# Optimization experiments

Hardware: AMD Instinct MI355X
Metric: run time of the kernel (lower is better)

Reference implementation:

```python
import jax, jax.numpy as jnp
import numpy as np

B, C, Q, E = 32, 1024, 128, 512

def setup_inputs() -> dict:
    key = jax.random.key(0)
    k1, k2, k3 = jax.random.split(key, 3)
    context = jax.random.normal(k1, (B, C, E), dtype=jnp.float32)
    question = jax.random.normal(k2, (B, Q, E), dtype=jnp.float32)
    # ws = [ws_q | ws_c | ws_m], matching cat([q, ctx, q*ctx]) order
    ws = jax.random.normal(k3, (3 * E,), dtype=jnp.float32) * (1.0 / np.sqrt(E))
    return {"context": context, "question": question, "ws": ws}

def reference(context, question, ws):
    ws_q, ws_c, ws_m = ws[:E], ws[E:2 * E], ws[2 * E:]
    # similarity[b,c,q] = ws_q.q[b,q] + ws_c.c[b,c] + ws_m.(q[b,q]*c[b,c])
    sim = (jnp.einsum('bqe,e->bq', question, ws_q)[:, None, :]
           + jnp.einsum('bce,e->bc', context, ws_c)[:, :, None]
           + jnp.einsum('bce,bqe,e->bcq', context, question, ws_m))  # (B,C,Q)
    c2q = jnp.einsum('bcq,bqe->bce', jax.nn.softmax(sim, axis=2), question)  # (B,C,E)
    q2c_w = jax.nn.softmax(jnp.max(sim, axis=2), axis=1)  # (B,C)
    q2c = jnp.einsum('bc,bce->be', q2c_w, context)[:, None, :]  # (B,1,E)
    return (c2q, q2c)
```

## Files before the change

kernel.cpp:

```cpp
#include <hip/hip_runtime.h>

#define BB 32
#define CC 1024
#define QQ 128
#define EE 512

typedef unsigned int uint32;
typedef unsigned short u16;
typedef __bf16 bf16x8 __attribute__((ext_vector_type(8)));
typedef float f32x4 __attribute__((ext_vector_type(4)));

#define QMF_OFF  (0u)
#define QTF_OFF  (4u<<20)
#define QDP_OFF  (8u<<20)
#define RDEN_OFF ((8u<<20)+(1u<<16))
#define MB_OFF   ((8u<<20)+(3u<<16))
#define SB_OFF   ((8u<<20)+(3u<<16)+4096u)
#define PVB_OFF  ((8u<<20)+(4u<<16))
#define P_OFF    (11u<<20)

__device__ __forceinline__ u16 bfc(float f){
  __bf16 h = (__bf16)f;
  return __builtin_bit_cast(u16, h);
}
__device__ __forceinline__ float bf2f(uint32 lo16){
  return __builtin_bit_cast(float, lo16 << 16);
}

__global__ __launch_bounds__(256) void k_prep(const float* __restrict__ q,
                                              const float* __restrict__ ws,
                                              unsigned char* __restrict__ wsp){
  const int b = blockIdx.x >> 2, et = blockIdx.x & 3, e0 = et*128;
  __shared__ u16 tm[128*136];
  __shared__ u16 tt[128*136];
  const int tid = threadIdx.x;
  float* qdp = (float*)(wsp + QDP_OFF) + (size_t)(b*4 + et)*128;
  #pragma unroll
  for (int i=0;i<16;i++){
    int id = tid + i*256;
    int qi = id >> 5;
    int el = (id & 31) << 2;
    float4 v = *(const float4*)(q + (size_t)(b*QQ+qi)*EE + e0 + el);
    float4 a = *(const float4*)(ws +          e0 + el);
    float4 c = *(const float4*)(ws +   EE +   e0 + el);
    float4 m = *(const float4*)(ws + 2*EE +   e0 + el);
    ushort4 um; um.x = bfc(v.x*m.x + c.x); um.y = bfc(v.y*m.y + c.y);
                um.z = bfc(v.z*m.z + c.z); um.w = bfc(v.w*m.w + c.w);
    *(ushort4*)&tm[qi*136 + el] = um;
    ushort4 ut; ut.x = bfc(v.x); ut.y = bfc(v.y); ut.z = bfc(v.z); ut.w = bfc(v.w);
    *(ushort4*)&tt[qi*136 + el] = ut;
    float d = v.x*a.x + v.y*a.y + v.z*a.z + v.w*a.w;
    d += __shfl_xor(d,1); d += __shfl_xor(d,2); d += __shfl_xor(d,4);
    d += __shfl_xor(d,8); d += __shfl_xor(d,16);
    if ((tid & 31) == 0) qdp[qi] = d;
  }
  __syncthreads();
  const int lane = tid & 63, wv = tid >> 6, l15 = lane & 15, l4 = lane >> 4;
  uint4* qmf = (uint4*)(wsp + QMF_OFF);
  uint4* qtf = (uint4*)(wsp + QTF_OFF);
  #pragma unroll
  for (int i=0;i<8;i++){
    int f = wv*8 + i;
    int kl = f >> 3, nf = f & 7;
    uint4 u = *(const uint4*)&tm[(nf*16 + l15)*136 + kl*32 + l4*8];
    qmf[(size_t)((b*16 + et*4 + kl)*8 + nf)*64 + lane] = u;
  }
  #pragma unroll
  for (int i=0;i<8;i++){
    int f = wv*8 + i;
    int ks2 = f >> 3, nl = f & 7, ne = et*8 + nl;
    uint32 x[4];
    #pragma unroll
    for (int p=0;p<4;p++){
      u16 t0 = tt[(ks2*32 + l4*8 + 2*p    )*136 + nl*16 + l15];
      u16 t1 = tt[(ks2*32 + l4*8 + 2*p + 1)*136 + nl*16 + l15];
      x[p] = (uint32)t0 | ((uint32)t1 << 16);
    }
    uint4 u; u.x = x[0]; u.y = x[1]; u.z = x[2]; u.w = x[3];
    qtf[(size_t)((b*4 + ks2)*32 + ne)*64 + lane] = u;
  }
}

__global__ __launch_bounds__(512, 4) void k_sim(const float* __restrict__ ctx,
                                                unsigned char* __restrict__ wsp){
  __shared__ __align__(16) unsigned char buf[32768];
  __shared__ float mx_s[32*8];
  __shared__ float sm_s[32*8];
  __shared__ float wrow_s[32];

  const int bid = blockIdx.x;
  const int sw  = (bid & 7)*128 + (bid >> 3);
  const int b   = sw >> 5;
  const int t   = sw & 31;
  const int tid = threadIdx.x;
  const int lane = tid & 63;
  const int w    = tid >> 6;
  const int l15  = lane & 15;
  const int l4   = lane >> 4;

  const float4* cb4 = (const float4*)(ctx + (size_t)(b*CC + t*32)*EE);
  float4 v[8];
  #pragma unroll
  for (int i=0;i<8;i++) v[i] = cb4[i*512 + tid];

  const uint4* qmf4 = (const uint4*)(wsp + QMF_OFF);
  bf16x8 a[16];
  #pragma unroll
  for (int ks=0;ks<16;ks++)
    a[ks] = __builtin_bit_cast(bf16x8, qmf4[(size_t)((b*16 + ks)*8 + w)*64 + lane]);
  float qdv[4];
  {
    const float* qdp = (const float*)(wsp + QDP_OFF) + (size_t)b*512;
    #pragma unroll
    for (int r=0;r<4;r++){
      const int qi = w*16 + l4*4 + r;
      qdv[r] = qdp[qi] + qdp[128+qi] + qdp[256+qi] + qdp[384+qi];
    }
  }

  {
    const int colb = (tid & 127)*8;
    #pragma unroll
    for (int i=0;i<8;i++){
      const int row = i*4 + (tid >> 7);
      uint2 u;
      u.x = (uint32)bfc(v[i].x) | ((uint32)bfc(v[i].y) << 16);
      u.y = (uint32)bfc(v[i].z) | ((uint32)bfc(v[i].w) << 16);
      *(uint2*)(buf + row*1024 + (colb ^ ((row & 7) << 4))) = u;
    }
  }
  __syncthreads();

  f32x4 acc[2];
  acc[0] = (f32x4){0.f,0.f,0.f,0.f};
  acc[1] = (f32x4){0.f,0.f,0.f,0.f};
  #pragma unroll
  for (int ks=0; ks<16; ks++){
    #pragma unroll
    for (int cc=0; cc<2; cc++){
      const int row = cc*16 + l15;
      bf16x8 bf = __builtin_bit_cast(bf16x8,
        *(const uint4*)(buf + row*1024 + ((ks*64 + l4*16) ^ ((row & 7) << 4))));
      acc[cc] = __builtin_amdgcn_mfma_f32_16x16x32_bf16(a[ks], bf, acc[cc], 0, 0, 0);
    }
  }

  {
    unsigned char* pgb = wsp + P_OFF
      + ((size_t)(b*64 + t*2)*4 + (w>>1))*1024
      + (((2*w + (l4>>1)) & 3)*16 + l15)*16 + (l4&1)*8;
    #pragma unroll
    for (int cc=0; cc<2; cc++){
      float m = -3.0e38f, s = 0.f;
      u16 hb[4];
      #pragma unroll
      for (int r=0;r<4;r++){
        float vv = fminf(acc[cc][r] + qdv[r], 80.f);
        m = fmaxf(m, vv);
        u16 h = bfc(__expf(vv));
        hb[r] = h;
        s += bf2f(h);
      }
      uint2 u; u.x = (uint32)hb[0] | ((uint32)hb[1]<<16);
               u.y = (uint32)hb[2] | ((uint32)hb[3]<<16);
      *(uint2*)(pgb + cc*4096) = u;
      m = fmaxf(m, __shfl_xor(m, 16)); m = fmaxf(m, __shfl_xor(m, 32));
      s += __shfl_xor(s, 16);          s += __shfl_xor(s, 32);
      if (l4 == 0){
        mx_s[(cc*16 + l15)*8 + w] = m;
        sm_s[(cc*16 + l15)*8 + w] = s;
      }
    }
  }
  __syncthreads();

  if (tid < 32){
    const float* sp = &sm_s[tid*8];
    float sum = sp[0]+sp[1]+sp[2]+sp[3]+sp[4]+sp[5]+sp[6]+sp[7];
    ((float*)(wsp + RDEN_OFF))[b*1024 + t*32 + tid] = 1.f/sum;
    const float* mp = &mx_s[tid*8];
    float mf = fmaxf(fmaxf(fmaxf(mp[0],mp[1]),fmaxf(mp[2],mp[3])),
                     fmaxf(fmaxf(mp[4],mp[5]),fmaxf(mp[6],mp[7])));
    float M = mf;
    M = fmaxf(M, __shfl_xor(M,1)); M = fmaxf(M, __shfl_xor(M,2));
    M = fmaxf(M, __shfl_xor(M,4)); M = fmaxf(M, __shfl_xor(M,8));
    M = fmaxf(M, __shfl_xor(M,16));
    float wr = __expf(mf - M);
    wrow_s[tid] = wr;
    float S = wr;
    S += __shfl_xor(S,1); S += __shfl_xor(S,2); S += __shfl_xor(S,4);
    S += __shfl_xor(S,8); S += __shfl_xor(S,16);
    if (tid == 0){
      ((float*)(wsp + MB_OFF))[b*32 + t] = M;
      ((float*)(wsp + SB_OFF))[b*32 + t] = S;
    }
  }
  __syncthreads();

  {
    float pv = 0.f;
    #pragma unroll
    for (int rr=0; rr<32; rr++){
      uint32 x = *(const u16*)(buf + rr*1024 + ((tid*2) ^ ((rr & 7) << 4)));
      pv = fmaf(wrow_s[rr], bf2f(x), pv);
    }
    ((float*)(wsp + PVB_OFF))[(size_t)(b*32 + t)*512 + tid] = pv;
  }
}

__global__ __launch_bounds__(256, 4) void k_out(unsigned char* __restrict__ wsp,
                                                float* __restrict__ out){
  __shared__ __align__(16) unsigned char qts[32768];

  const int bid = blockIdx.x;
  const int sw  = (bid & 7)*256 + (bid >> 3);
  const int b   = sw >> 6;
  const int rr  = sw & 63;
  const int ct  = rr >> 2;
  const int et  = rr & 3;
  const int tid = threadIdx.x;
  const int lane = tid & 63;
  const int w    = tid >> 6;
  const int l15  = lane & 15;
  const int l4   = lane >> 4;

  const unsigned char* qtfb = wsp + QTF_OFF + (size_t)b*131072;
  #pragma unroll
  for (int j=0;j<8;j++){
    __builtin_amdgcn_global_load_lds(
      (const __attribute__((address_space(1))) uint32*)
        (qtfb + (size_t)(w*32 + et*8 + j)*1024 + lane*16),
      (__attribute__((address_space(3))) uint32*)(qts + (w*8 + j)*1024), 16, 0, 0);
  }

  bf16x8 pa[4];
  #pragma unroll
  for (int k2=0;k2<4;k2++)
    pa[k2] = __builtin_bit_cast(bf16x8,
      *(const uint4*)(wsp + P_OFF + ((size_t)(b*64 + ct*4 + w)*4 + k2)*1024 + lane*16));
  float rden[4];
  {
    const float* rg = (const float*)(wsp + RDEN_OFF) + b*1024 + ct*64 + w*16;
    #pragma unroll
    for (int r=0;r<4;r++) rden[r] = rg[l4*4 + r];
  }
  __syncthreads();

  f32x4 acc2[8];
  #pragma unroll
  for (int n=0;n<8;n++) acc2[n] = (f32x4){0.f,0.f,0.f,0.f};
  #pragma unroll
  for (int k2=0;k2<4;k2++){
    #pragma unroll
    for (int n=0;n<8;n++){
      bf16x8 bq = __builtin_bit_cast(bf16x8,
        *(const uint4*)(qts + (k2*8 + n)*1024 + lane*16));
      acc2[n] = __builtin_amdgcn_mfma_f32_16x16x32_bf16(pa[k2], bq, acc2[n], 0, 0, 0);
    }
  }

  float* ob = out + (size_t)(b*CC + ct*64 + w*16)*EE + et*128;
  #pragma unroll
  for (int n=0;n<8;n++){
    #pragma unroll
    for (int r=0;r<4;r++)
      ob[(size_t)(l4*4 + r)*EE + n*16 + l15] = acc2[n][r]*rden[r];
  }
}

__global__ __launch_bounds__(256) void k_fin(unsigned char* __restrict__ wsp,
                                             float* __restrict__ out){
  const int b = blockIdx.x;
  __shared__ float sc_s[32];
  __shared__ float dinv_s;
  const int tid = threadIdx.x;
  if (tid < 32){
    float Mk = ((const float*)(wsp + MB_OFF))[b*32 + tid];
    float Sk = ((const float*)(wsp + SB_OFF))[b*32 + tid];
    float M = Mk;
    M = fmaxf(M, __shfl_xor(M,1)); M = fmaxf(M, __shfl_xor(M,2));
    M = fmaxf(M, __shfl_xor(M,4)); M = fmaxf(M, __shfl_xor(M,8));
    M = fmaxf(M, __shfl_xor(M,16));
    float ev = __expf(Mk - M);
    float d = ev*Sk;
    d += __shfl_xor(d,1); d += __shfl_xor(d,2); d += __shfl_xor(d,4);
    d += __shfl_xor(d,8); d += __shfl_xor(d,16);
    sc_s[tid] = ev;
    if (tid == 0) dinv_s = 1.f/d;
  }
  __syncthreads();
  const float* pvb = (const float*)(wsp + PVB_OFF) + (size_t)b*32*512;
  float a0 = 0.f, a1 = 0.f;
  #pragma unroll
  for (int k=0;k<32;k++){
    float s = sc_s[k];
    a0 = fmaf(s, pvb[k*512 + tid],       a0);
    a1 = fmaf(s, pvb[k*512 + tid + 256], a1);
  }
  size_t base = (size_t)BB*CC*EE + (size_t)b*EE;
  float di = dinv_s;
  out[base + tid]       = a0*di;
  out[base + tid + 256] = a1*di;
}

extern "C" void kernel_launch(void* const* d_in, const int* in_sizes, int n_in,
                              void* d_out, int out_size, void* d_ws, size_t ws_size,
                              hipStream_t stream){
  const float* ctx = (const float*)d_in[0];
  const float* q   = (const float*)d_in[1];
  const float* ws  = (const float*)d_in[2];
  float* out = (float*)d_out;
  unsigned char* wsp = (unsigned char*)d_ws;

  k_prep<<<dim3(BB*4), dim3(256), 0, stream>>>(q, ws, wsp);
  k_sim <<<dim3(1024), dim3(512), 0, stream>>>(ctx, wsp);
  k_out <<<dim3(2048), dim3(256), 0, stream>>>(wsp, out);
  k_fin <<<dim3(BB),   dim3(256), 0, stream>>>(wsp, out);
}
```

Before: 53.56 us.

## Halve k_sim context tile to 16 rows and fold k_fin into k_out

```diff
diff --git a/kernel.cpp b/kernel.cpp
--- a/kernel.cpp
+++ b/kernel.cpp
@@ -13,11 +13,11 @@
 #define QMF_OFF  (0u)
 #define QTF_OFF  (4u<<20)
 #define QDP_OFF  (8u<<20)
-#define RDEN_OFF ((8u<<20)+(1u<<16))
-#define MB_OFF   ((8u<<20)+(3u<<16))
-#define SB_OFF   ((8u<<20)+(3u<<16)+4096u)
-#define PVB_OFF  ((8u<<20)+(4u<<16))
-#define P_OFF    (11u<<20)
+#define RDEN_OFF ((8u<<20)+(64u<<10))
+#define MB_OFF   ((8u<<20)+(192u<<10))
+#define SB_OFF   ((8u<<20)+(200u<<10))
+#define PVB_OFF  ((8u<<20)+(256u<<10))
+#define P_OFF    (13u<<20)
 
 __device__ __forceinline__ u16 bfc(float f){
   __bf16 h = (__bf16)f;
@@ -83,31 +83,26 @@
 
 __global__ __launch_bounds__(512, 4) void k_sim(const float* __restrict__ ctx,
                                                 unsigned char* __restrict__ wsp){
-  __shared__ __align__(16) unsigned char buf[32768];
-  __shared__ float mx_s[32*8];
-  __shared__ float sm_s[32*8];
-  __shared__ float wrow_s[32];
+  __shared__ __align__(16) unsigned char buf[16384];
+  __shared__ float mx_s[16*8];
+  __shared__ float sm_s[16*8];
+  __shared__ float wrow_s[16];
 
   const int bid = blockIdx.x;
-  const int sw  = (bid & 7)*128 + (bid >> 3);
-  const int b   = sw >> 5;
-  const int t   = sw & 31;
+  const int sw  = (bid & 7)*256 + (bid >> 3);
+  const int b   = sw >> 6;
+  const int t   = sw & 63;
   const int tid = threadIdx.x;
   const int lane = tid & 63;
   const int w    = tid >> 6;
   const int l15  = lane & 15;
   const int l4   = lane >> 4;
 
-  const float4* cb4 = (const float4*)(ctx + (size_t)(b*CC + t*32)*EE);
-  float4 v[8];
-  #pragma unroll
-  for (int i=0;i<8;i++) v[i] = cb4[i*512 + tid];
-
-  const uint4* qmf4 = (const uint4*)(wsp + QMF_OFF);
-  bf16x8 a[16];
-  #pragma unroll
-  for (int ks=0;ks<16;ks++)
-    a[ks] = __builtin_bit_cast(bf16x8, qmf4[(size_t)((b*16 + ks)*8 + w)*64 + lane]);
+  const float4* cb4 = (const float4*)(ctx + (size_t)(b*CC + t*16)*EE);
+  float4 v[4];
+  #pragma unroll
+  for (int i=0;i<4;i++) v[i] = cb4[i*512 + tid];
+
   float qdv[4];
   {
     const float* qdp = (const float*)(wsp + QDP_OFF) + (size_t)b*512;
@@ -121,7 +116,7 @@
   {
     const int colb = (tid & 127)*8;
     #pragma unroll
-    for (int i=0;i<8;i++){
+    for (int i=0;i<4;i++){
       const int row = i*4 + (tid >> 7);
       uint2 u;
       u.x = (uint32)bfc(v[i].x) | ((uint32)bfc(v[i].y) << 16);
@@ -131,68 +126,56 @@
   }
   __syncthreads();
 
-  f32x4 acc[2];
-  acc[0] = (f32x4){0.f,0.f,0.f,0.f};
-  acc[1] = (f32x4){0.f,0.f,0.f,0.f};
+  const uint4* qmf4 = (const uint4*)(wsp + QMF_OFF);
+  f32x4 acc = (f32x4){0.f,0.f,0.f,0.f};
   #pragma unroll
   for (int ks=0; ks<16; ks++){
-    #pragma unroll
-    for (int cc=0; cc<2; cc++){
-      const int row = cc*16 + l15;
-      bf16x8 bf = __builtin_bit_cast(bf16x8,
-        *(const uint4*)(buf + row*1024 + ((ks*64 + l4*16) ^ ((row & 7) << 4))));
-      acc[cc] = __builtin_amdgcn_mfma_f32_16x16x32_bf16(a[ks], bf, acc[cc], 0, 0, 0);
-    }
-  }
-
-  {
-    unsigned char* pgb = wsp + P_OFF
-      + ((size_t)(b*64 + t*2)*4 + (w>>1))*1024
-      + (((2*w + (l4>>1)) & 3)*16 + l15)*16 + (l4&1)*8;
-    #pragma unroll
-    for (int cc=0; cc<2; cc++){
-      float m = -3.0e38f, s = 0.f;
-      u16 hb[4];
-      #pragma unroll
-      for (int r=0;r<4;r++){
-        float vv = fminf(acc[cc][r] + qdv[r], 80.f);
-        m = fmaxf(m, vv);
-        u16 h = bfc(__expf(vv));
-        hb[r] = h;
-        s += bf2f(h);
-      }
-      uint2 u; u.x = (uint32)hb[0] | ((uint32)hb[1]<<16);
-               u.y = (uint32)hb[2] | ((uint32)hb[3]<<16);
-      *(uint2*)(pgb + cc*4096) = u;
-      m = fmaxf(m, __shfl_xor(m, 16)); m = fmaxf(m, __shfl_xor(m, 32));
-      s += __shfl_xor(s, 16);          s += __shfl_xor(s, 32);
-      if (l4 == 0){
-        mx_s[(cc*16 + l15)*8 + w] = m;
-        sm_s[(cc*16 + l15)*8 + w] = s;
-      }
-    }
-  }
-  __syncthreads();
-
-  if (tid < 32){
+    bf16x8 a = __builtin_bit_cast(bf16x8, qmf4[(size_t)((b*16 + ks)*8 + w)*64 + lane]);
+    bf16x8 bf = __builtin_bit_cast(bf16x8,
+      *(const uint4*)(buf + l15*1024 + ((ks*64 + l4*16) ^ ((l15 & 7) << 4))));
+    acc = __builtin_amdgcn_mfma_f32_16x16x32_bf16(a, bf, acc, 0, 0, 0);
+  }
+
+  {
+    float m = -3.0e38f, s = 0.f;
+    u16 hb[4];
+    #pragma unroll
+    for (int r=0;r<4;r++){
+      float vv = fminf(acc[r] + qdv[r], 80.f);
+      m = fmaxf(m, vv);
+      u16 h = bfc(__expf(vv));
+      hb[r] = h;
+      s += bf2f(h);
+    }
+    uint2 u; u.x = (uint32)hb[0] | ((uint32)hb[1]<<16);
+             u.y = (uint32)hb[2] | ((uint32)hb[3]<<16);
+    *(uint2*)(wsp + P_OFF
+      + ((size_t)(b*64 + t)*4 + (w>>1))*1024
+      + (((2*w + (l4>>1)) & 3)*16 + l15)*16 + (l4&1)*8) = u;
+    m = fmaxf(m, __shfl_xor(m, 16)); m = fmaxf(m, __shfl_xor(m, 32));
+    s += __shfl_xor(s, 16);          s += __shfl_xor(s, 32);
+    if (l4 == 0){ mx_s[l15*8 + w] = m; sm_s[l15*8 + w] = s; }
+  }
+  __syncthreads();
+
+  if (tid < 16){
     const float* sp = &sm_s[tid*8];
     float sum = sp[0]+sp[1]+sp[2]+sp[3]+sp[4]+sp[5]+sp[6]+sp[7];
-    ((float*)(wsp + RDEN_OFF))[b*1024 + t*32 + tid] = 1.f/sum;
+    ((float*)(wsp + RDEN_OFF))[b*1024 + t*16 + tid] = 1.f/sum;
     const float* mp = &mx_s[tid*8];
     float mf = fmaxf(fmaxf(fmaxf(mp[0],mp[1]),fmaxf(mp[2],mp[3])),
                      fmaxf(fmaxf(mp[4],mp[5]),fmaxf(mp[6],mp[7])));
     float M = mf;
     M = fmaxf(M, __shfl_xor(M,1)); M = fmaxf(M, __shfl_xor(M,2));
     M = fmaxf(M, __shfl_xor(M,4)); M = fmaxf(M, __shfl_xor(M,8));
-    M = fmaxf(M, __shfl_xor(M,16));
     float wr = __expf(mf - M);
     wrow_s[tid] = wr;
     float S = wr;
-    S += __shfl_xor(S,1); S += __shfl_xor(S,2); S += __shfl_xor(S,4);
-    S += __shfl_xor(S,8); S += __shfl_xor(S,16);
+    S += __shfl_xor(S,1); S += __shfl_xor(S,2);
+    S += __shfl_xor(S,4); S += __shfl_xor(S,8);
     if (tid == 0){
-      ((float*)(wsp + MB_OFF))[b*32 + t] = M;
-      ((float*)(wsp + SB_OFF))[b*32 + t] = S;
+      ((float*)(wsp + MB_OFF))[b*64 + t] = M;
+      ((float*)(wsp + SB_OFF))[b*64 + t] = S;
     }
   }
   __syncthreads();
@@ -200,25 +183,60 @@
   {
     float pv = 0.f;
     #pragma unroll
-    for (int rr=0; rr<32; rr++){
+    for (int rr=0; rr<16; rr++){
       uint32 x = *(const u16*)(buf + rr*1024 + ((tid*2) ^ ((rr & 7) << 4)));
       pv = fmaf(wrow_s[rr], bf2f(x), pv);
     }
-    ((float*)(wsp + PVB_OFF))[(size_t)(b*32 + t)*512 + tid] = pv;
+    ((float*)(wsp + PVB_OFF))[(size_t)(b*64 + t)*512 + tid] = pv;
   }
 }
 
 __global__ __launch_bounds__(256, 4) void k_out(unsigned char* __restrict__ wsp,
                                                 float* __restrict__ out){
   __shared__ __align__(16) unsigned char qts[32768];
+  __shared__ float sc_s[64];
+  __shared__ float dinv_s;
 
   const int bid = blockIdx.x;
+  const int tid = threadIdx.x;
+
+  if (bid >= 2048){
+    const int b = bid - 2048;
+    if (tid < 64){
+      float Mk = ((const float*)(wsp + MB_OFF))[b*64 + tid];
+      float Sk = ((const float*)(wsp + SB_OFF))[b*64 + tid];
+      float M = Mk;
+      M = fmaxf(M, __shfl_xor(M,1));  M = fmaxf(M, __shfl_xor(M,2));
+      M = fmaxf(M, __shfl_xor(M,4));  M = fmaxf(M, __shfl_xor(M,8));
+      M = fmaxf(M, __shfl_xor(M,16)); M = fmaxf(M, __shfl_xor(M,32));
+      float ev = __expf(Mk - M);
+      float d = ev*Sk;
+      d += __shfl_xor(d,1);  d += __shfl_xor(d,2);  d += __shfl_xor(d,4);
+      d += __shfl_xor(d,8);  d += __shfl_xor(d,16); d += __shfl_xor(d,32);
+      sc_s[tid] = ev;
+      if (tid == 0) dinv_s = 1.f/d;
+    }
+    __syncthreads();
+    const float* pvb = (const float*)(wsp + PVB_OFF) + (size_t)b*64*512;
+    float a0 = 0.f, a1 = 0.f;
+    #pragma unroll 8
+    for (int k=0;k<64;k++){
+      float s = sc_s[k];
+      a0 = fmaf(s, pvb[(size_t)k*512 + tid],       a0);
+      a1 = fmaf(s, pvb[(size_t)k*512 + tid + 256], a1);
+    }
+    size_t base = (size_t)BB*CC*EE + (size_t)b*EE;
+    float di = dinv_s;
+    out[base + tid]       = a0*di;
+    out[base + tid + 256] = a1*di;
+    return;
+  }
+
   const int sw  = (bid & 7)*256 + (bid >> 3);
   const int b   = sw >> 6;
   const int rr  = sw & 63;
   const int ct  = rr >> 2;
   const int et  = rr & 3;
-  const int tid = threadIdx.x;
   const int lane = tid & 63;
   const int w    = tid >> 6;
   const int l15  = lane & 15;
@@ -266,41 +284,6 @@
     for (int r=0;r<4;r++)
       ob[(size_t)(l4*4 + r)*EE + n*16 + l15] = acc2[n][r]*rden[r];
   }
-}
-
-__global__ __launch_bounds__(256) void k_fin(unsigned char* __restrict__ wsp,
-                                             float* __restrict__ out){
-  const int b = blockIdx.x;
-  __shared__ float sc_s[32];
-  __shared__ float dinv_s;
-  const int tid = threadIdx.x;
-  if (tid < 32){
-    float Mk = ((const float*)(wsp + MB_OFF))[b*32 + tid];
-    float Sk = ((const float*)(wsp + SB_OFF))[b*32 + tid];
-    float M = Mk;
-    M = fmaxf(M, __shfl_xor(M,1)); M = fmaxf(M, __shfl_xor(M,2));
-    M = fmaxf(M, __shfl_xor(M,4)); M = fmaxf(M, __shfl_xor(M,8));
-    M = fmaxf(M, __shfl_xor(M,16));
-    float ev = __expf(Mk - M);
-    float d = ev*Sk;
-    d += __shfl_xor(d,1); d += __shfl_xor(d,2); d += __shfl_xor(d,4);
-    d += __shfl_xor(d,8); d += __shfl_xor(d,16);
-    sc_s[tid] = ev;
-    if (tid == 0) dinv_s = 1.f/d;
-  }
-  __syncthreads();
-  const float* pvb = (const float*)(wsp + PVB_OFF) + (size_t)b*32*512;
-  float a0 = 0.f, a1 = 0.f;
-  #pragma unroll
-  for (int k=0;k<32;k++){
-    float s = sc_s[k];
-    a0 = fmaf(s, pvb[k*512 + tid],       a0);
-    a1 = fmaf(s, pvb[k*512 + tid + 256], a1);
-  }
-  size_t base = (size_t)BB*CC*EE + (size_t)b*EE;
-  float di = dinv_s;
-  out[base + tid]       = a0*di;
-  out[base + tid + 256] = a1*di;
 }
 
 extern "C" void kernel_launch(void* const* d_in, const int* in_sizes, int n_in,
@@ -312,8 +295,7 @@
   float* out = (float*)d_out;
   unsigned char* wsp = (unsigned char*)d_ws;
 
-  k_prep<<<dim3(BB*4), dim3(256), 0, stream>>>(q, ws, wsp);
-  k_sim <<<dim3(1024), dim3(512), 0, stream>>>(ctx, wsp);
-  k_out <<<dim3(2048), dim3(256), 0, stream>>>(wsp, out);
-  k_fin <<<dim3(BB),   dim3(256), 0, stream>>>(wsp, out);
-}
+  k_prep<<<dim3(BB*4),    dim3(256), 0, stream>>>(q, ws, wsp);
+  k_sim <<<dim3(2048),    dim3(512), 0, stream>>>(ctx, wsp);
+  k_out <<<dim3(2048+32), dim3(256), 0, stream>>>(wsp, out);
+}
```

Measured after the change: 54.68 us. 2.1% more time.
